# Kernel optimization log

Measured on AMD Instinct MI355X. Metric: run time of the kernel, lower is better.

## Reference

```python
import jax, jax.numpy as jnp
import numpy as np

B, D = 4096, 16384
PHASE_WEIGHT = 2.0
CIRCLE_FACTOR = 1.0
RECT_FACTOR = 1.3


def setup_inputs() -> dict:
    key = jax.random.key(0)
    k1, k2, k3, k4, k5 = jax.random.split(key, 5)
    return {
        "phase_sin_pred": jax.random.normal(k1, (B, D), dtype=jnp.float32),
        "phase_cos_pred": jax.random.normal(k2, (B, D), dtype=jnp.float32),
        "phase_sin_true": jax.random.normal(k3, (B, D), dtype=jnp.float32),
        "phase_cos_true": jax.random.normal(k4, (B, D), dtype=jnp.float32),
        "shape_types": jax.random.uniform(k5, (B,), dtype=jnp.float32),
    }


def reference(phase_sin_pred, phase_cos_pred, phase_sin_true, phase_cos_true, shape_types):
    # Per-sample MSE over trailing dims (MSELoss(reduction='none') then .mean() per sample)
    sin_mse = jnp.mean((phase_sin_pred - phase_sin_true) ** 2, axis=-1)  # [B]
    cos_mse = jnp.mean((phase_cos_pred - phase_cos_true) ** 2, axis=-1)  # [B]
    # Python loop -> vectorized: factor chosen per sample by shape type
    factor = jnp.where(shape_types < 0.5, CIRCLE_FACTOR, RECT_FACTOR)  # [B]
    weighted = jnp.mean((sin_mse + cos_mse) * factor)
    return PHASE_WEIGHT * weighted
```

## Files before the change

kernel.cpp:

```cpp
#include <hip/hip_runtime.h>


constexpr int B_DIM = 4096;
constexpr int D_DIM = 16384;
constexpr int NVEC_SHIFT = 12;
constexpr long long NVEC = (long long)B_DIM * D_DIM / 4;
constexpr int NBLOCKS = 2048;
constexpr int NTHREADS = 256;

__global__ __launch_bounds__(NTHREADS) void phase_loss_partial(
    const float4* __restrict__ sp, const float4* __restrict__ cp,
    const float4* __restrict__ st, const float4* __restrict__ ct,
    const float* __restrict__ shape_types, float* __restrict__ partials)
{
    float acc = 0.0f;
    const long long stride = (long long)gridDim.x * blockDim.x;
    for (long long i = (long long)blockIdx.x * blockDim.x + threadIdx.x; i < NVEC; i += stride) {
        const int row = (int)(i >> NVEC_SHIFT);
        const float f = (shape_types[row] < 0.5f) ? 1.0f : 1.3f;
        const float4 a = sp[i];
        const float4 b = st[i];
        const float4 c = cp[i];
        const float4 d = ct[i];
        const float dx0 = a.x - b.x, dx1 = a.y - b.y, dx2 = a.z - b.z, dx3 = a.w - b.w;
        const float dy0 = c.x - d.x, dy1 = c.y - d.y, dy2 = c.z - d.z, dy3 = c.w - d.w;
        float s = dx0 * dx0;
        s = fmaf(dx1, dx1, s);
        s = fmaf(dx2, dx2, s);
        s = fmaf(dx3, dx3, s);
        s = fmaf(dy0, dy0, s);
        s = fmaf(dy1, dy1, s);
        s = fmaf(dy2, dy2, s);
        s = fmaf(dy3, dy3, s);
        acc = fmaf(f, s, acc);
    }

    #pragma unroll
    for (int off = 32; off > 0; off >>= 1)
        acc += __shfl_down(acc, off, 64);

    __shared__ float wsum[NTHREADS / 64];
    const int lane = threadIdx.x & 63;
    const int wave = threadIdx.x >> 6;
    if (lane == 0) wsum[wave] = acc;
    __syncthreads();
    if (threadIdx.x == 0) {
        float t = wsum[0] + wsum[1] + wsum[2] + wsum[3];
        partials[blockIdx.x] = t;
    }
}

__global__ __launch_bounds__(NTHREADS) void phase_loss_final(
    const float* __restrict__ partials, float* __restrict__ out)
{
    float acc = 0.0f;
    for (int i = threadIdx.x; i < NBLOCKS; i += NTHREADS)
        acc += partials[i];

    #pragma unroll
    for (int off = 32; off > 0; off >>= 1)
        acc += __shfl_down(acc, off, 64);

    __shared__ float wsum[NTHREADS / 64];
    const int lane = threadIdx.x & 63;
    const int wave = threadIdx.x >> 6;
    if (lane == 0) wsum[wave] = acc;
    __syncthreads();
    if (threadIdx.x == 0) {
        const float total = wsum[0] + wsum[1] + wsum[2] + wsum[3];
        const float scale = 2.0f / ((float)B_DIM * (float)D_DIM);
        out[0] = scale * total;
    }
}

extern "C" void kernel_launch(void* const* d_in, const int* in_sizes, int n_in,
                              void* d_out, int out_size, void* d_ws, size_t ws_size,
                              hipStream_t stream) {
    const float4* sp = (const float4*)d_in[0];
    const float4* cp = (const float4*)d_in[1];
    const float4* st = (const float4*)d_in[2];
    const float4* ct = (const float4*)d_in[3];
    const float* shape_types = (const float*)d_in[4];
    float* out = (float*)d_out;
    float* partials = (float*)d_ws;

    phase_loss_partial<<<NBLOCKS, NTHREADS, 0, stream>>>(sp, cp, st, ct, shape_types, partials);
    phase_loss_final<<<1, NTHREADS, 0, stream>>>(partials, out);
}
```

Measured before the change: 202.9 us.

## Map each block to a half row with unrolled loads and hoisted factor

Replaces the grid-stride loop with a fixed mapping where each of 8192 blocks reduces half of one row. The per-row shape factor is then loaded once per block instead of on every iteration. The inner loop is fully unrolled with two independent accumulators, so eight float4 loads are in flight per step, which raises memory-level parallelism on this bandwidth-bound reduction. In exchange there are four times as many partials for the final kernel to sum, and the launch now has many short-lived blocks instead of persistent ones.

```diff
diff --git a/kernel.cpp b/kernel.cpp
--- a/kernel.cpp
+++ b/kernel.cpp
@@ -3,51 +3,61 @@
 
 constexpr int B_DIM = 4096;
 constexpr int D_DIM = 16384;
-constexpr int NVEC_SHIFT = 12;
-constexpr long long NVEC = (long long)B_DIM * D_DIM / 4;
-constexpr int NBLOCKS = 2048;
+constexpr int ROW_VECS = D_DIM / 4;
+constexpr int HALF_VECS = ROW_VECS / 2;
+constexpr int NBLOCKS = B_DIM * 2;
 constexpr int NTHREADS = 256;
+constexpr int ITERS = HALF_VECS / NTHREADS;
+
+__device__ __forceinline__ float sq_diff_acc(float4 a, float4 b, float s) {
+    s = fmaf(a.x - b.x, a.x - b.x, s);
+    s = fmaf(a.y - b.y, a.y - b.y, s);
+    s = fmaf(a.z - b.z, a.z - b.z, s);
+    s = fmaf(a.w - b.w, a.w - b.w, s);
+    return s;
+}
 
 __global__ __launch_bounds__(NTHREADS) void phase_loss_partial(
     const float4* __restrict__ sp, const float4* __restrict__ cp,
     const float4* __restrict__ st, const float4* __restrict__ ct,
     const float* __restrict__ shape_types, float* __restrict__ partials)
 {
-    float acc = 0.0f;
-    const long long stride = (long long)gridDim.x * blockDim.x;
-    for (long long i = (long long)blockIdx.x * blockDim.x + threadIdx.x; i < NVEC; i += stride) {
-        const int row = (int)(i >> NVEC_SHIFT);
-        const float f = (shape_types[row] < 0.5f) ? 1.0f : 1.3f;
-        const float4 a = sp[i];
-        const float4 b = st[i];
-        const float4 c = cp[i];
-        const float4 d = ct[i];
-        const float dx0 = a.x - b.x, dx1 = a.y - b.y, dx2 = a.z - b.z, dx3 = a.w - b.w;
-        const float dy0 = c.x - d.x, dy1 = c.y - d.y, dy2 = c.z - d.z, dy3 = c.w - d.w;
-        float s = dx0 * dx0;
-        s = fmaf(dx1, dx1, s);
-        s = fmaf(dx2, dx2, s);
-        s = fmaf(dx3, dx3, s);
-        s = fmaf(dy0, dy0, s);
-        s = fmaf(dy1, dy1, s);
-        s = fmaf(dy2, dy2, s);
-        s = fmaf(dy3, dy3, s);
-        acc = fmaf(f, s, acc);
+    const int row = blockIdx.x >> 1;
+    const float f = (shape_types[row] < 0.5f) ? 1.0f : 1.3f;
+    const long long base = (long long)blockIdx.x * HALF_VECS;
+
+    float s0 = 0.0f, s1 = 0.0f;
+    #pragma unroll
+    for (int it = 0; it < ITERS; it += 2) {
+        const long long idx0 = base + it * NTHREADS + threadIdx.x;
+        const long long idx1 = idx0 + NTHREADS;
+        const float4 a0 = sp[idx0];
+        const float4 b0 = st[idx0];
+        const float4 c0 = cp[idx0];
+        const float4 d0 = ct[idx0];
+        const float4 a1 = sp[idx1];
+        const float4 b1 = st[idx1];
+        const float4 c1 = cp[idx1];
+        const float4 d1 = ct[idx1];
+
+        s0 = sq_diff_acc(a0, b0, s0);
+        s0 = sq_diff_acc(c0, d0, s0);
+        s1 = sq_diff_acc(a1, b1, s1);
+        s1 = sq_diff_acc(c1, d1, s1);
     }
+    float block_acc = f * (s0 + s1);
 
     #pragma unroll
     for (int off = 32; off > 0; off >>= 1)
-        acc += __shfl_down(acc, off, 64);
+        block_acc += __shfl_down(block_acc, off, 64);
 
     __shared__ float wsum[NTHREADS / 64];
     const int lane = threadIdx.x & 63;
     const int wave = threadIdx.x >> 6;
-    if (lane == 0) wsum[wave] = acc;
+    if (lane == 0) wsum[wave] = block_acc;
     __syncthreads();
-    if (threadIdx.x == 0) {
-        float t = wsum[0] + wsum[1] + wsum[2] + wsum[3];
-        partials[blockIdx.x] = t;
-    }
+    if (threadIdx.x == 0)
+        partials[blockIdx.x] = wsum[0] + wsum[1] + wsum[2] + wsum[3];
 }
 
 __global__ __launch_bounds__(NTHREADS) void phase_loss_final(
```

Result: faster. 189.6 us (-6.5%).
